# Kernel optimization log

Hardware: AMD Instinct MI355X
Metric: run time of the kernel (lower is better)

## Reference

```python
import jax, jax.numpy as jnp
import numpy as np

N_POINTS = 1 << 20
N_LEVELS = 16
F_PER_LVL = 2
LOG2_T = 19
T = 1 << LOG2_T
BASE_RES = 16
PER_LEVEL_SCALE = float(np.exp2(np.log2(2048.0 / 16.0) / (N_LEVELS - 1)))
# 8 trilinear corner offsets [8,3]
OFFSETS = np.stack(np.meshgrid(*([np.array([0, 1])] * 3), indexing='ij'), axis=-1).reshape(8, 3)
PRIMES = np.array([1, 2654435761, 805459861], dtype=np.uint32)  # tcnn spatial hash primes


def _level_params(l):
    # tcnn: grid_scale = 2^(l*log2(s)) * base - 1 ; resolution = ceil(scale)+1
    scale = np.exp2(l * np.log2(PER_LEVEL_SCALE)) * BASE_RES - 1.0
    res = int(np.ceil(scale)) + 1
    return float(scale), res


def hash_encode(x, table):
    """x: [N,3] in [0,1]; table: [L,T,F]. Returns [N, L*F]."""
    offs = jnp.asarray(OFFSETS)                     # [8,3] int32
    primes = jnp.asarray(PRIMES)                    # [3] uint32
    feats = []
    for l in range(N_LEVELS):
        scale, res = _level_params(l)
        pos = x * scale + 0.5                       # [N,3]
        pos_grid = jnp.floor(pos)
        w = pos - pos_grid                          # [N,3] interp weights
        c0 = pos_grid.astype(jnp.int32)             # [N,3]
        corners = c0[None, :, :] + offs[:, None, :]  # [8,N,3]
        if res ** 3 <= T:
            # dense indexing for coarse levels (fits in hashmap)
            cc = jnp.clip(corners, 0, res - 1)
            idx = cc[..., 0] + cc[..., 1] * res + cc[..., 2] * (res * res)
        else:
            cu = corners.astype(jnp.uint32)
            h = (cu[..., 0] * primes[0]) ^ (cu[..., 1] * primes[1]) ^ (cu[..., 2] * primes[2])
            idx = (h & jnp.uint32(T - 1)).astype(jnp.int32)
        f = table[l][idx]                           # [8,N,F] gather
        # trilinear weights: prod over dims of (w if corner bit else 1-w)
        wc = jnp.prod(jnp.where(offs[:, None, :] == 1, w[None], 1.0 - w[None]), axis=-1)  # [8,N]
        feats.append(jnp.sum(wc[..., None] * f, axis=0))  # [N,F]
    return jnp.concatenate(feats, axis=-1)          # [N, 32]


def _softplus10(z):
    return jax.nn.softplus(10.0 * z) / 10.0


def setup_inputs() -> dict:
    key = jax.random.key(0)
    k = jax.random.split(key, 6)
    x = jax.random.uniform(k[0], (N_POINTS, 3), dtype=jnp.float32)
    table = jax.random.normal(k[1], (N_LEVELS, T, F_PER_LVL), dtype=jnp.float32) * 1e-2
    w1 = jax.random.normal(k[2], (64, 32), dtype=jnp.float32) * 0.1
    w2 = jax.random.normal(k[3], (64, 64), dtype=jnp.float32) * 0.1
    w3 = jax.random.normal(k[4], (64, 64), dtype=jnp.float32) * 0.1
    w4 = jax.random.normal(k[5], (1, 64), dtype=jnp.float32) * 0.1
    return {"x": x, "table": table, "w1": w1, "w2": w2, "w3": w3, "w4": w4}


def reference(x, table, w1, w2, w3, w4):
    enc = hash_encode(x, table)                     # [N,32]
    h = _softplus10(enc @ w1.T)
    h = _softplus10(h @ w2.T)
    h = _softplus10(h @ w3.T)
    sdf = h @ w4.T                                  # [N,1]
    return sdf
```

## Files before the change

kernel.cpp:

```cpp
#include <hip/hip_runtime.h>
#include <cmath>

#define T_SIZE (1u << 19)
#define CB 512
#define NBLK 128
#define RCAP 3584

typedef _Float16 h8 __attribute__((ext_vector_type(8)));
typedef _Float16 h4 __attribute__((ext_vector_type(4)));
typedef _Float16 h2 __attribute__((ext_vector_type(2)));
typedef float f4 __attribute__((ext_vector_type(4)));

struct Levels {
    float scale[16];
    int   res[16];
    unsigned dense_mask;
};

__device__ __forceinline__ float softplus10(float z) {
    float e = __builtin_amdgcn_exp2f(fminf(z * 14.426950408889634f, 126.0f));
    return __builtin_amdgcn_logf(1.0f + e) * 0.069314718055994531f;
}

__global__ __launch_bounds__(256) void convert_kernel(
    const float2* __restrict__ t, h2* __restrict__ o, int total4,
    const float* __restrict__ w1, const float* __restrict__ w2,
    const float* __restrict__ w3, _Float16* __restrict__ wh)
{
    int i = blockIdx.x * 256 + threadIdx.x;
    if (i < total4) {
        const float2* src = t + (size_t)i * 4;
        h8 r;
#pragma unroll
        for (int j = 0; j < 4; ++j) {
            float2 v = src[j];
            r[2 * j]     = (_Float16)v.x;
            r[2 * j + 1] = (_Float16)v.y;
        }
        *(h8*)(o + (size_t)i * 4) = r;
    } else {
        int k = i - total4;
        if (k < 10240) {
            float v = (k < 2048) ? w1[k] : (k < 6144) ? w2[k - 2048] : w3[k - 6144];
            wh[k] = (_Float16)v;
        }
    }
}

__device__ __forceinline__ unsigned spread3(unsigned v) {
    v &= 1023u;
    v = (v | (v << 16)) & 0x030000FFu;
    v = (v | (v << 8))  & 0x0300F00Fu;
    v = (v | (v << 4))  & 0x030C30C3u;
    v = (v | (v << 2))  & 0x09249249u;
    return v;
}

__device__ __forceinline__ unsigned morton_key(float px, float py, float pz) {
    unsigned qx = (unsigned)fminf(fmaxf(px, 0.f) * 32.f, 31.f);
    unsigned qy = (unsigned)fminf(fmaxf(py, 0.f) * 32.f, 31.f);
    unsigned qz = (unsigned)fminf(fmaxf(pz, 0.f) * 32.f, 31.f);
    return (spread3(qx) << 2) | (spread3(qy) << 1) | spread3(qz);
}

__global__ __launch_bounds__(256) void hist_kernel(
    const float* __restrict__ xs, unsigned* __restrict__ M, int N)
{
    __shared__ unsigned h[CB];
    for (int t = threadIdx.x; t < CB; t += 256) h[t] = 0u;
    __syncthreads();
    const int per = N / NBLK;
    const int s = blockIdx.x * per;
    for (int i = s + threadIdx.x; i < s + per; i += 256) {
        unsigned k = morton_key(xs[3 * i], xs[3 * i + 1], xs[3 * i + 2]) >> 6;
        atomicAdd(&h[k], 1u);
    }
    __syncthreads();
    for (int t = threadIdx.x; t < CB; t += 256)
        M[t * NBLK + blockIdx.x] = h[t];
}

__global__ __launch_bounds__(1024) void scan_kernel(
    const unsigned* __restrict__ M, unsigned* __restrict__ Ms)
{
    __shared__ unsigned tmp[1024];
    const int t = threadIdx.x;
    const int PER = (CB * NBLK) / 1024;
    unsigned s = 0;
    for (int j = 0; j < PER; ++j) s += M[t * PER + j];
    tmp[t] = s;
    __syncthreads();
    for (int d = 1; d < 1024; d <<= 1) {
        unsigned v = (t >= d) ? tmp[t - d] : 0u;
        __syncthreads();
        tmp[t] += v;
        __syncthreads();
    }
    unsigned run = (t > 0) ? tmp[t - 1] : 0u;
    for (int j = 0; j < PER; ++j) {
        unsigned v = M[t * PER + j];
        Ms[t * PER + j] = run;
        run += v;
    }
}

__global__ __launch_bounds__(256) void cscatter_kernel(
    const float* __restrict__ xs, const unsigned* __restrict__ Ms,
    float4* __restrict__ sx4, int N)
{
    __shared__ unsigned cur[CB];
    for (int t = threadIdx.x; t < CB; t += 256)
        cur[t] = Ms[t * NBLK + blockIdx.x];
    __syncthreads();
    const int per = N / NBLK;
    const int s = blockIdx.x * per;
    for (int i = s + threadIdx.x; i < s + per; i += 256) {
        float px = xs[3 * i], py = xs[3 * i + 1], pz = xs[3 * i + 2];
        unsigned k = morton_key(px, py, pz) >> 6;
        unsigned pos = atomicAdd(&cur[k], 1u);
        sx4[pos] = make_float4(px, py, pz, __uint_as_float((unsigned)i));
    }
}

__global__ __launch_bounds__(256) void refine_kernel(
    float4* __restrict__ sx4, const unsigned* __restrict__ Ms, int N)
{
    __shared__ float4 pts[RCAP];
    __shared__ unsigned h[64], base[64];
    const int b = blockIdx.x;
    const unsigned s = Ms[b * NBLK];
    const unsigned e = (b == CB - 1) ? (unsigned)N : Ms[(b + 1) * NBLK];
    const unsigned cnt = e - s;
    if (cnt > RCAP) return;
    if (threadIdx.x < 64) h[threadIdx.x] = 0u;
    __syncthreads();
    for (unsigned i = threadIdx.x; i < cnt; i += 256) {
        float4 q = sx4[s + i];
        pts[i] = q;
        unsigned k = morton_key(q.x, q.y, q.z) & 63u;
        atomicAdd(&h[k], 1u);
    }
    __syncthreads();
    if (threadIdx.x == 0) {
        unsigned a = 0;
        for (int j = 0; j < 64; ++j) { base[j] = a; a += h[j]; }
    }
    __syncthreads();
    if (threadIdx.x < 64) h[threadIdx.x] = 0u;
    __syncthreads();
    for (unsigned i = threadIdx.x; i < cnt; i += 256) {
        float4 q = pts[i];
        unsigned k = morton_key(q.x, q.y, q.z) & 63u;
        unsigned r = base[k] + atomicAdd(&h[k], 1u);
        sx4[s + r] = q;
    }
}

__device__ __forceinline__ void gather_pair(
    const h2* __restrict__ tl, unsigned i0, unsigned i1,
    float2& v0, float2& v1)
{
    unsigned g = i0 & ~3u;
    union { h8 v; uint4 u; } cv;
    cv.v = *(const h8*)(tl + g);
    unsigned p0 = i0 & 3u;
    unsigned a01 = (p0 & 1u) ? cv.u.y : cv.u.x;
    unsigned a23 = (p0 & 1u) ? cv.u.w : cv.u.z;
    unsigned e0  = (p0 & 2u) ? a23 : a01;
    unsigned e1;
    if ((i1 & ~3u) == g) {
        unsigned p1 = i1 & 3u;
        unsigned b01 = (p1 & 1u) ? cv.u.y : cv.u.x;
        unsigned b23 = (p1 & 1u) ? cv.u.w : cv.u.z;
        e1 = (p1 & 2u) ? b23 : b01;
    } else {
        e1 = *(const unsigned*)(tl + i1);
    }
    h2 c0 = __builtin_bit_cast(h2, e0);
    h2 c1 = __builtin_bit_cast(h2, e1);
    v0 = make_float2((float)c0[0], (float)c0[1]);
    v1 = make_float2((float)c1[0], (float)c1[1]);
}

__device__ __forceinline__ h2 encode_point(
    float px, float py, float pz, float s, int res, bool dense,
    const h2* __restrict__ tl)
{
    float fx = px * s + 0.5f, fy = py * s + 0.5f, fz = pz * s + 0.5f;
    float gx = floorf(fx), gy = floorf(fy), gz = floorf(fz);
    float wx = fx - gx, wy = fy - gy, wz = fz - gz;
    int cx = (int)gx, cy = (int)gy, cz = (int)gz;

    float2 vx0[4], vx1[4];
    if (dense) {
        int r1 = res - 1;
        int x0 = min(cx, r1), x1 = min(cx + 1, r1);
        int y0 = min(cy, r1), y1 = min(cy + 1, r1);
        int z0 = min(cz, r1), z1 = min(cz + 1, r1);
        int rr = res * res;
        int bases[4] = {y0 * res + z0 * rr, y0 * res + z1 * rr,
                        y1 * res + z0 * rr, y1 * res + z1 * rr};
#pragma unroll
        for (int j = 0; j < 4; ++j)
            gather_pair(tl, (unsigned)(x0 + bases[j]), (unsigned)(x1 + bases[j]),
                        vx0[j], vx1[j]);
    } else {
        unsigned hy0 = (unsigned)cy * 2654435761u, hy1 = (unsigned)(cy + 1) * 2654435761u;
        unsigned hz0 = (unsigned)cz * 805459861u,  hz1 = (unsigned)(cz + 1) * 805459861u;
        unsigned Y[4] = {hy0 ^ hz0, hy0 ^ hz1, hy1 ^ hz0, hy1 ^ hz1};
        const unsigned M = T_SIZE - 1;
#pragma unroll
        for (int j = 0; j < 4; ++j)
            gather_pair(tl, ((unsigned)cx ^ Y[j]) & M,
                        ((unsigned)(cx + 1) ^ Y[j]) & M, vx0[j], vx1[j]);
    }

    float wx0 = 1.f - wx, wy0 = 1.f - wy, wz0 = 1.f - wz;
    float wyz[4] = {wy0 * wz0, wy0 * wz, wy * wz0, wy * wz};
    float f0 = 0.f, f1 = 0.f;
#pragma unroll
    for (int j = 0; j < 4; ++j) {
        float w0 = wx0 * wyz[j], w1 = wx * wyz[j];
        f0 += w0 * vx0[j].x + w1 * vx1[j].x;
        f1 += w0 * vx0[j].y + w1 * vx1[j].y;
    }
    h2 r; r[0] = (_Float16)f0; r[1] = (_Float16)f1;
    return r;
}

__global__ __launch_bounds__(256) void encode_kernel(
    const float* __restrict__ xs, const h2* __restrict__ table,
    h2* __restrict__ enc2, Levels lv, int lbase, int N)
{
    __shared__ float sx[768];
    const int i0 = blockIdx.x * 256;
    for (int t = threadIdx.x; t < 768; t += 256) sx[t] = xs[(size_t)i0 * 3 + t];
    __syncthreads();

    const int l = lbase + blockIdx.y;
    const int i = i0 + threadIdx.x;
    if (i >= N) return;
    h2 r = encode_point(sx[threadIdx.x * 3], sx[threadIdx.x * 3 + 1],
                        sx[threadIdx.x * 3 + 2], lv.scale[l], lv.res[l],
                        (lv.dense_mask >> l) & 1u, table + (size_t)l * T_SIZE);
    enc2[(size_t)l * N + i] = r;
}

__global__ __launch_bounds__(256) void encode_kernel_sorted(
    const float4* __restrict__ xs4, const h2* __restrict__ table,
    h2* __restrict__ enc2, Levels lv, int lbase, int N)
{
    const int i = blockIdx.x * 256 + threadIdx.x;
    if (i >= N) return;
    const int l = lbase + blockIdx.y;
    float4 q = xs4[i];
    h2 r = encode_point(q.x, q.y, q.z, lv.scale[l], lv.res[l],
                        (lv.dense_mask >> l) & 1u, table + (size_t)l * T_SIZE);
    enc2[(size_t)l * N + i] = r;
}

template <typename WT>
__device__ __forceinline__ h8 load_frag8(const WT* p) {
    if constexpr (sizeof(WT) == 2) {
        return *(const h8*)p;
    } else {
        h8 r;
#pragma unroll
        for (int j = 0; j < 8; ++j) r[j] = (_Float16)p[j];
        return r;
    }
}

template <typename WT, bool LOCAL, bool SORTED>
__global__ __launch_bounds__(256, 3) void fused_kernel(
    const float* __restrict__ xs, const float4* __restrict__ xs4,
    const h2* __restrict__ table16, const h2* __restrict__ enc2,
    const WT* __restrict__ w1, const WT* __restrict__ w2,
    const WT* __restrict__ w3, const float* __restrict__ w4,
    float* __restrict__ out, Levels lv, int N)
{
    constexpr int AR = 72;
    __shared__ __align__(16) char smem[4 * 9216];
    __shared__ float sx[768];

    const int tid  = threadIdx.x;
    const int wave = tid >> 6;
    const int lane = tid & 63;
    const int lrow = lane & 15;
    const int quad = lane >> 4;
    const int base = blockIdx.x * 256;
    char* wmem = smem + wave * 9216;
    const f4 zero = {0.f, 0.f, 0.f, 0.f};

    float px, py, pz;
    unsigned oi = 0;
    if constexpr (SORTED) {
        float4 q = xs4[base + tid];
        px = q.x; py = q.y; pz = q.z;
        oi = __float_as_uint(q.w);
    } else {
        for (int t = tid; t < 768; t += 256) sx[t] = xs[(size_t)base * 3 + t];
        __syncthreads();
        px = sx[tid * 3]; py = sx[tid * 3 + 1]; pz = sx[tid * 3 + 2];
    }
    const int p = tid & 63;

    if (LOCAL) {
#pragma unroll
        for (int l = 5; l < 15; ++l) {
            h2 v = enc2[(size_t)l * N + base + tid];
            *(h2*)(wmem + ((l >> 2) << 10) + (p << 4) + ((l & 3) << 2)) = v;
        }
        const int LMAP[6] = {0, 1, 2, 3, 4, 15};
#pragma unroll 2
        for (int s6 = 0; s6 < 6; ++s6) {
            const int l = LMAP[s6];
            h2 v = encode_point(px, py, pz, lv.scale[l], lv.res[l],
                                (lv.dense_mask >> l) & 1u,
                                table16 + (size_t)l * T_SIZE);
            *(h2*)(wmem + ((l >> 2) << 10) + (p << 4) + ((l & 3) << 2)) = v;
        }
    } else {
#pragma unroll
        for (int l = 0; l < 16; ++l) {
            h2 v = enc2[(size_t)l * N + base + tid];
            *(h2*)(wmem + ((l >> 2) << 10) + (p << 4) + ((l & 3) << 2)) = v;
        }
    }

    asm volatile("" ::: "memory");

    h8 aW1[4];
#pragma unroll
    for (int tm = 0; tm < 4; ++tm)
        aW1[tm] = load_frag8(w1 + (tm * 16 + lrow) * 32 + quad * 8);
    h8 aW2[4][2], aW3[4][2];
#pragma unroll
    for (int tm = 0; tm < 4; ++tm)
#pragma unroll
        for (int km = 0; km < 2; ++km) {
            aW2[tm][km] = load_frag8(w2 + (tm * 16 + lrow) * 64 + km * 32 + quad * 8);
            aW3[tm][km] = load_frag8(w3 + (tm * 16 + lrow) * 64 + km * 32 + quad * 8);
        }
    h4 w4q[4];
#pragma unroll
    for (int tm = 0; tm < 4; ++tm)
#pragma unroll
        for (int r = 0; r < 4; ++r) w4q[tm][r] = (_Float16)w4[tm * 16 + quad * 4 + r];

    h8 bin[4];
#pragma unroll
    for (int t = 0; t < 4; ++t)
        bin[t] = *(const h8*)(wmem + (quad << 10) + ((t * 16 + lrow) << 4));

    _Float16* wAct = (_Float16*)wmem;

#pragma unroll
    for (int t = 0; t < 4; ++t) {
        const int arow = (t * 16 + lrow) * AR;
#pragma unroll
        for (int tm = 0; tm < 4; ++tm) {
            f4 acc = __builtin_amdgcn_mfma_f32_16x16x32_f16(aW1[tm], bin[t], zero, 0, 0, 0);
            h4 pk;
#pragma unroll
            for (int r = 0; r < 4; ++r) pk[r] = (_Float16)softplus10(acc[r]);
            *(h4*)&wAct[arow + tm * 16 + quad * 4] = pk;
        }
    }

#pragma unroll
    for (int t = 0; t < 4; ++t) {
        const int arow = (t * 16 + lrow) * AR;
        h8 b0 = *(const h8*)&wAct[arow + quad * 8];
        h8 b1 = *(const h8*)&wAct[arow + 32 + quad * 8];
        f4 accs[4];
#pragma unroll
        for (int tm = 0; tm < 4; ++tm) {
            f4 acc = __builtin_amdgcn_mfma_f32_16x16x32_f16(aW2[tm][0], b0, zero, 0, 0, 0);
            acc     = __builtin_amdgcn_mfma_f32_16x16x32_f16(aW2[tm][1], b1, acc,  0, 0, 0);
            accs[tm] = acc;
        }
#pragma unroll
        for (int tm = 0; tm < 4; ++tm) {
            h4 pk;
#pragma unroll
            for (int r = 0; r < 4; ++r) pk[r] = (_Float16)softplus10(accs[tm][r]);
            *(h4*)&wAct[arow + tm * 16 + quad * 4] = pk;
        }
    }

#pragma unroll
    for (int t = 0; t < 4; ++t) {
        const int arow = (t * 16 + lrow) * AR;
        h8 b0 = *(const h8*)&wAct[arow + quad * 8];
        h8 b1 = *(const h8*)&wAct[arow + 32 + quad * 8];
        float sum = 0.f;
#pragma unroll
        for (int tm = 0; tm < 4; ++tm) {
            f4 acc = __builtin_amdgcn_mfma_f32_16x16x32_f16(aW3[tm][0], b0, zero, 0, 0, 0);
            acc     = __builtin_amdgcn_mfma_f32_16x16x32_f16(aW3[tm][1], b1, acc,  0, 0, 0);
#pragma unroll
            for (int r = 0; r < 4; ++r)
                sum += (float)w4q[tm][r] * softplus10(acc[r]);
        }
        sum += __shfl_xor(sum, 16, 64);
        sum += __shfl_xor(sum, 32, 64);
        if constexpr (SORTED) {
            unsigned t_oi = __shfl(oi, t * 16 + lrow, 64);
            if (quad == 0) out[t_oi] = sum;
        } else {
            if (quad == 0)
                out[base + wave * 64 + t * 16 + lrow] = sum;
        }
    }
}

__global__ __launch_bounds__(256) void encode_kernel_f32(
    const float* __restrict__ xs, const float2* __restrict__ table,
    h2* __restrict__ enc2, Levels lv, int N)
{
    const int i = blockIdx.x * 256 + threadIdx.x;
    const int l = blockIdx.y;
    if (i >= N) return;
    float px = xs[3 * i], py = xs[3 * i + 1], pz = xs[3 * i + 2];
    float s = lv.scale[l];
    int res = lv.res[l];
    float fx = px * s + 0.5f, fy = py * s + 0.5f, fz = pz * s + 0.5f;
    float gx = floorf(fx), gy = floorf(fy), gz = floorf(fz);
    float wx = fx - gx, wy = fy - gy, wz = fz - gz;
    int cx = (int)gx, cy = (int)gy, cz = (int)gz;
    unsigned idx[8];
    if ((lv.dense_mask >> l) & 1u) {
        int r1 = res - 1;
        int x0 = min(cx, r1), x1 = min(cx + 1, r1);
        int y0 = min(cy, r1), y1 = min(cy + 1, r1);
        int z0 = min(cz, r1), z1 = min(cz + 1, r1);
        int rr = res * res;
        idx[0] = x0 + y0 * res + z0 * rr; idx[1] = x0 + y0 * res + z1 * rr;
        idx[2] = x0 + y1 * res + z0 * rr; idx[3] = x0 + y1 * res + z1 * rr;
        idx[4] = x1 + y0 * res + z0 * rr; idx[5] = x1 + y0 * res + z1 * rr;
        idx[6] = x1 + y1 * res + z0 * rr; idx[7] = x1 + y1 * res + z1 * rr;
    } else {
        unsigned hx0 = (unsigned)cx, hx1 = (unsigned)(cx + 1);
        unsigned hy0 = (unsigned)cy * 2654435761u, hy1 = (unsigned)(cy + 1) * 2654435761u;
        unsigned hz0 = (unsigned)cz * 805459861u,  hz1 = (unsigned)(cz + 1) * 805459861u;
        idx[0] = (hx0^hy0^hz0) & (T_SIZE-1); idx[1] = (hx0^hy0^hz1) & (T_SIZE-1);
        idx[2] = (hx0^hy1^hz0) & (T_SIZE-1); idx[3] = (hx0^hy1^hz1) & (T_SIZE-1);
        idx[4] = (hx1^hy0^hz0) & (T_SIZE-1); idx[5] = (hx1^hy0^hz1) & (T_SIZE-1);
        idx[6] = (hx1^hy1^hz0) & (T_SIZE-1); idx[7] = (hx1^hy1^hz1) & (T_SIZE-1);
    }
    const float2* tl = table + (size_t)l * T_SIZE;
    float wx0 = 1.f - wx, wy0 = 1.f - wy, wz0 = 1.f - wz;
    float wcs[8] = {wx0*wy0*wz0, wx0*wy0*wz, wx0*wy*wz0, wx0*wy*wz,
                    wx*wy0*wz0,  wx*wy0*wz,  wx*wy*wz0,  wx*wy*wz};
    float f0 = 0.f, f1 = 0.f;
#pragma unroll
    for (int c = 0; c < 8; ++c) {
        float2 v = tl[idx[c]];
        f0 += wcs[c] * v.x; f1 += wcs[c] * v.y;
    }
    h2 r; r[0] = (_Float16)f0; r[1] = (_Float16)f1;
    enc2[(size_t)l * N + i] = r;
}

extern "C" void kernel_launch(void* const* d_in, const int* in_sizes, int n_in,
                              void* d_out, int out_size, void* d_ws, size_t ws_size,
                              hipStream_t stream) {
    const float* x     = (const float*)d_in[0];
    const float* table = (const float*)d_in[1];
    const float* w1    = (const float*)d_in[2];
    const float* w2    = (const float*)d_in[3];
    const float* w3    = (const float*)d_in[4];
    const float* w4    = (const float*)d_in[5];
    float* out = (float*)d_out;
    const int N = in_sizes[0] / 3;

    Levels lv;
    lv.dense_mask = 0;
    const double pls = exp2(log2(2048.0 / 16.0) / 15.0);
    const double lg  = log2(pls);
    for (int l = 0; l < 16; ++l) {
        double sc = exp2((double)l * lg) * 16.0 - 1.0;
        int res = (int)ceil(sc) + 1;
        lv.scale[l] = (float)sc;
        lv.res[l]   = res;
        if ((long long)res * res * res <= (long long)T_SIZE) lv.dense_mask |= (1u << l);
    }

    const size_t encBytes   = (size_t)16 * N * 4;
    const size_t tableBytes = (size_t)16 * T_SIZE * 4;
    const size_t whBytes    = 32768;
    const size_t sx4Bytes   = (size_t)N * 16;
    const size_t mBytes     = (size_t)CB * NBLK * 4;
    h2* enc2 = (h2*)d_ws;

    const int ptBlocks = (N + 255) / 256;

    if (ws_size >= encBytes + tableBytes + whBytes + sx4Bytes + 2 * mBytes
        && (N % NBLK) == 0) {
        h2* table16    = (h2*)((char*)d_ws + encBytes);
        _Float16* wh   = (_Float16*)((char*)d_ws + encBytes + tableBytes);
        float4* sx4    = (float4*)((char*)d_ws + encBytes + tableBytes + whBytes);
        unsigned* M    = (unsigned*)((char*)d_ws + encBytes + tableBytes + whBytes + sx4Bytes);
        unsigned* Ms   = M + (size_t)CB * NBLK;

        const int total4 = 16 * T_SIZE / 4;
        const int convBlocks = (total4 + 10240 + 255) / 256;
        hipLaunchKernelGGL(convert_kernel, dim3(convBlocks), dim3(256), 0, stream,
                           (const float2*)table, table16, total4, w1, w2, w3, wh);

        hipLaunchKernelGGL(hist_kernel, dim3(NBLK), dim3(256), 0, stream, x, M, N);
        hipLaunchKernelGGL(scan_kernel, dim3(1), dim3(1024), 0, stream, M, Ms);
        hipLaunchKernelGGL(cscatter_kernel, dim3(NBLK), dim3(256), 0, stream,
                           x, Ms, sx4, N);
        hipLaunchKernelGGL(refine_kernel, dim3(CB), dim3(256), 0, stream,
                           sx4, Ms, N);

        hipLaunchKernelGGL(encode_kernel_sorted, dim3(ptBlocks, 10), dim3(256), 0, stream,
                           (const float4*)sx4, (const h2*)table16, enc2, lv, 5, N);
        hipLaunchKernelGGL((fused_kernel<_Float16, true, true>), dim3(ptBlocks), dim3(256),
                           0, stream, x, (const float4*)sx4, (const h2*)table16,
                           (const h2*)enc2, wh, wh + 2048, wh + 6144, w4, out, lv, N);
    } else if (ws_size >= encBytes + tableBytes + whBytes) {
        h2* table16 = (h2*)((char*)d_ws + encBytes);
        _Float16* wh = (_Float16*)((char*)d_ws + encBytes + tableBytes);
        const int total4 = 16 * T_SIZE / 4;
        const int convBlocks = (total4 + 10240 + 255) / 256;
        hipLaunchKernelGGL(convert_kernel, dim3(convBlocks), dim3(256), 0, stream,
                           (const float2*)table, table16, total4, w1, w2, w3, wh);
        hipLaunchKernelGGL(encode_kernel, dim3(ptBlocks, 10), dim3(256), 0, stream,
                           x, (const h2*)table16, enc2, lv, 5, N);
        hipLaunchKernelGGL((fused_kernel<_Float16, true, false>), dim3(ptBlocks), dim3(256),
                           0, stream, x, (const float4*)nullptr, (const h2*)table16,
                           (const h2*)enc2, wh, wh + 2048, wh + 6144, w4, out, lv, N);
    } else {
        hipLaunchKernelGGL(encode_kernel_f32, dim3(ptBlocks, 16), dim3(256), 0, stream,
                           x, (const float2*)table, enc2, lv, N);
        hipLaunchKernelGGL((fused_kernel<float, false, false>), dim3(ptBlocks), dim3(256),
                           0, stream, x, (const float4*)nullptr, (const h2*)nullptr,
                           (const h2*)enc2, w1, w2, w3, w4, out, lv, N);
    }
}
```

Before: 451.6 us.

## Fuse histogram into convert kernel and stage coarse scatter through LDS

New measurement: 481.3 us. 1.07x slower.

```diff
diff --git a/kernel.cpp b/kernel.cpp
--- a/kernel.cpp
+++ b/kernel.cpp
@@ -3,7 +3,7 @@
 
 #define T_SIZE (1u << 19)
 #define CB 512
-#define NBLK 128
+#define NBLK 512
 #define RCAP 3584
 
 typedef _Float16 h8 __attribute__((ext_vector_type(8)));
@@ -20,31 +20,6 @@
 __device__ __forceinline__ float softplus10(float z) {
     float e = __builtin_amdgcn_exp2f(fminf(z * 14.426950408889634f, 126.0f));
     return __builtin_amdgcn_logf(1.0f + e) * 0.069314718055994531f;
-}
-
-__global__ __launch_bounds__(256) void convert_kernel(
-    const float2* __restrict__ t, h2* __restrict__ o, int total4,
-    const float* __restrict__ w1, const float* __restrict__ w2,
-    const float* __restrict__ w3, _Float16* __restrict__ wh)
-{
-    int i = blockIdx.x * 256 + threadIdx.x;
-    if (i < total4) {
-        const float2* src = t + (size_t)i * 4;
-        h8 r;
-#pragma unroll
-        for (int j = 0; j < 4; ++j) {
-            float2 v = src[j];
-            r[2 * j]     = (_Float16)v.x;
-            r[2 * j + 1] = (_Float16)v.y;
-        }
-        *(h8*)(o + (size_t)i * 4) = r;
-    } else {
-        int k = i - total4;
-        if (k < 10240) {
-            float v = (k < 2048) ? w1[k] : (k < 6144) ? w2[k - 2048] : w3[k - 6144];
-            wh[k] = (_Float16)v;
-        }
-    }
 }
 
 __device__ __forceinline__ unsigned spread3(unsigned v) {
@@ -63,31 +38,58 @@
     return (spread3(qx) << 2) | (spread3(qy) << 1) | spread3(qz);
 }
 
-__global__ __launch_bounds__(256) void hist_kernel(
-    const float* __restrict__ xs, unsigned* __restrict__ M, int N)
-{
-    __shared__ unsigned h[CB];
-    for (int t = threadIdx.x; t < CB; t += 256) h[t] = 0u;
-    __syncthreads();
-    const int per = N / NBLK;
-    const int s = blockIdx.x * per;
-    for (int i = s + threadIdx.x; i < s + per; i += 256) {
-        unsigned k = morton_key(xs[3 * i], xs[3 * i + 1], xs[3 * i + 2]) >> 6;
-        atomicAdd(&h[k], 1u);
-    }
-    __syncthreads();
-    for (int t = threadIdx.x; t < CB; t += 256)
-        M[t * NBLK + blockIdx.x] = h[t];
+__global__ __launch_bounds__(256) void convert_kernel(
+    const float2* __restrict__ t, h2* __restrict__ o, int total4,
+    const float* __restrict__ w1, const float* __restrict__ w2,
+    const float* __restrict__ w3, _Float16* __restrict__ wh,
+    const float* __restrict__ xs, unsigned short* __restrict__ M, int N)
+{
+    const int histStart = (total4 + 10240 + 255) >> 8;
+    if ((int)blockIdx.x >= histStart) {
+        __shared__ unsigned h[CB];
+        const int blk = blockIdx.x - histStart;
+        for (int t2 = threadIdx.x; t2 < CB; t2 += 256) h[t2] = 0u;
+        __syncthreads();
+        const int s = blk * 2048;
+#pragma unroll
+        for (int j = 0; j < 8; ++j) {
+            int i = s + threadIdx.x + j * 256;
+            unsigned k = morton_key(xs[3 * i], xs[3 * i + 1], xs[3 * i + 2]) >> 6;
+            atomicAdd(&h[k], 1u);
+        }
+        __syncthreads();
+        for (int t2 = threadIdx.x; t2 < CB; t2 += 256)
+            M[t2 * NBLK + blk] = (unsigned short)h[t2];
+        return;
+    }
+    int i = blockIdx.x * 256 + threadIdx.x;
+    if (i < total4) {
+        const float2* src = t + (size_t)i * 4;
+        h8 r;
+#pragma unroll
+        for (int j = 0; j < 4; ++j) {
+            float2 v = src[j];
+            r[2 * j]     = (_Float16)v.x;
+            r[2 * j + 1] = (_Float16)v.y;
+        }
+        *(h8*)(o + (size_t)i * 4) = r;
+    } else {
+        int k = i - total4;
+        if (k < 10240) {
+            float v = (k < 2048) ? w1[k] : (k < 6144) ? w2[k - 2048] : w3[k - 6144];
+            wh[k] = (_Float16)v;
+        }
+    }
 }
 
 __global__ __launch_bounds__(1024) void scan_kernel(
-    const unsigned* __restrict__ M, unsigned* __restrict__ Ms)
+    const unsigned short* __restrict__ M, unsigned* __restrict__ Ms)
 {
     __shared__ unsigned tmp[1024];
     const int t = threadIdx.x;
-    const int PER = (CB * NBLK) / 1024;
+    const int PERS = (CB * NBLK) / 1024;
     unsigned s = 0;
-    for (int j = 0; j < PER; ++j) s += M[t * PER + j];
+    for (int j = 0; j < PERS; ++j) s += M[t * PERS + j];
     tmp[t] = s;
     __syncthreads();
     for (int d = 1; d < 1024; d <<= 1) {
@@ -97,9 +99,9 @@
         __syncthreads();
     }
     unsigned run = (t > 0) ? tmp[t - 1] : 0u;
-    for (int j = 0; j < PER; ++j) {
-        unsigned v = M[t * PER + j];
-        Ms[t * PER + j] = run;
+    for (int j = 0; j < PERS; ++j) {
+        unsigned v = M[t * PERS + j];
+        Ms[t * PERS + j] = run;
         run += v;
     }
 }
@@ -108,18 +110,53 @@
     const float* __restrict__ xs, const unsigned* __restrict__ Ms,
     float4* __restrict__ sx4, int N)
 {
-    __shared__ unsigned cur[CB];
-    for (int t = threadIdx.x; t < CB; t += 256)
-        cur[t] = Ms[t * NBLK + blockIdx.x];
-    __syncthreads();
-    const int per = N / NBLK;
-    const int s = blockIdx.x * per;
-    for (int i = s + threadIdx.x; i < s + per; i += 256) {
+    __shared__ float4  pts[2048];
+    __shared__ unsigned gp[2048];
+    __shared__ unsigned lh[CB];
+    __shared__ unsigned lbase[CB];
+    __shared__ unsigned tmp[256];
+    const int tid = threadIdx.x;
+    const int blk = blockIdx.x;
+    for (int t2 = tid; t2 < CB; t2 += 256) lh[t2] = 0u;
+    __syncthreads();
+    const int s = blk * 2048;
+    float4  myp[8];
+    unsigned myk[8];
+#pragma unroll
+    for (int j = 0; j < 8; ++j) {
+        int i = s + tid + j * 256;
         float px = xs[3 * i], py = xs[3 * i + 1], pz = xs[3 * i + 2];
-        unsigned k = morton_key(px, py, pz) >> 6;
-        unsigned pos = atomicAdd(&cur[k], 1u);
-        sx4[pos] = make_float4(px, py, pz, __uint_as_float((unsigned)i));
-    }
+        myp[j] = make_float4(px, py, pz, __uint_as_float((unsigned)i));
+        myk[j] = morton_key(px, py, pz) >> 6;
+        atomicAdd(&lh[myk[j]], 1u);
+    }
+    __syncthreads();
+    unsigned a0 = lh[2 * tid], a1 = lh[2 * tid + 1];
+    tmp[tid] = a0 + a1;
+    __syncthreads();
+    for (int d = 1; d < 256; d <<= 1) {
+        unsigned v = (tid >= d) ? tmp[tid - d] : 0u;
+        __syncthreads();
+        tmp[tid] += v;
+        __syncthreads();
+    }
+    unsigned eb = (tid > 0) ? tmp[tid - 1] : 0u;
+    lbase[2 * tid] = eb;
+    lbase[2 * tid + 1] = eb + a0;
+    __syncthreads();
+    lh[2 * tid] = 0u; lh[2 * tid + 1] = 0u;
+    __syncthreads();
+#pragma unroll
+    for (int j = 0; j < 8; ++j) {
+        unsigned k = myk[j];
+        unsigned r = atomicAdd(&lh[k], 1u);
+        unsigned slot = lbase[k] + r;
+        pts[slot] = myp[j];
+        gp[slot] = Ms[k * NBLK + blk] + r;
+    }
+    __syncthreads();
+    for (int j = tid; j < 2048; j += 256)
+        sx4[gp[j]] = pts[j];
 }
 
 __global__ __launch_bounds__(256) void refine_kernel(
@@ -160,20 +197,13 @@
     const h2* __restrict__ tl, unsigned i0, unsigned i1,
     float2& v0, float2& v1)
 {
-    unsigned g = i0 & ~3u;
-    union { h8 v; uint4 u; } cv;
-    cv.v = *(const h8*)(tl + g);
-    unsigned p0 = i0 & 3u;
-    unsigned a01 = (p0 & 1u) ? cv.u.y : cv.u.x;
-    unsigned a23 = (p0 & 1u) ? cv.u.w : cv.u.z;
-    unsigned e0  = (p0 & 2u) ? a23 : a01;
-    unsigned e1;
-    if ((i1 & ~3u) == g) {
-        unsigned p1 = i1 & 3u;
-        unsigned b01 = (p1 & 1u) ? cv.u.y : cv.u.x;
-        unsigned b23 = (p1 & 1u) ? cv.u.w : cv.u.z;
-        e1 = (p1 & 2u) ? b23 : b01;
-    } else {
+    unsigned e0, e1;
+    if ((i0 ^ i1) == 1u) {
+        uint2 both = *(const uint2*)(tl + (i0 & ~1u));
+        e0 = (i0 & 1u) ? both.y : both.x;
+        e1 = (i0 & 1u) ? both.x : both.y;
+    } else {
+        e0 = *(const unsigned*)(tl + i0);
         e1 = *(const unsigned*)(tl + i1);
     }
     h2 c0 = __builtin_bit_cast(h2, e0);
@@ -491,25 +521,23 @@
     const size_t tableBytes = (size_t)16 * T_SIZE * 4;
     const size_t whBytes    = 32768;
     const size_t sx4Bytes   = (size_t)N * 16;
-    const size_t mBytes     = (size_t)CB * NBLK * 4;
     h2* enc2 = (h2*)d_ws;
 
     const int ptBlocks = (N + 255) / 256;
 
-    if (ws_size >= encBytes + tableBytes + whBytes + sx4Bytes + 2 * mBytes
-        && (N % NBLK) == 0) {
+    if (ws_size >= encBytes + tableBytes + whBytes + sx4Bytes
+        && N == NBLK * 2048) {
         h2* table16    = (h2*)((char*)d_ws + encBytes);
         _Float16* wh   = (_Float16*)((char*)d_ws + encBytes + tableBytes);
         float4* sx4    = (float4*)((char*)d_ws + encBytes + tableBytes + whBytes);
-        unsigned* M    = (unsigned*)((char*)d_ws + encBytes + tableBytes + whBytes + sx4Bytes);
-        unsigned* Ms   = M + (size_t)CB * NBLK;
+        unsigned short* M = (unsigned short*)d_ws;
+        unsigned* Ms      = (unsigned*)((char*)d_ws + 1024 * 1024);
 
         const int total4 = 16 * T_SIZE / 4;
         const int convBlocks = (total4 + 10240 + 255) / 256;
-        hipLaunchKernelGGL(convert_kernel, dim3(convBlocks), dim3(256), 0, stream,
-                           (const float2*)table, table16, total4, w1, w2, w3, wh);
-
-        hipLaunchKernelGGL(hist_kernel, dim3(NBLK), dim3(256), 0, stream, x, M, N);
+        hipLaunchKernelGGL(convert_kernel, dim3(convBlocks + NBLK), dim3(256), 0,
+                           stream, (const float2*)table, table16, total4,
+                           w1, w2, w3, wh, x, M, N);
         hipLaunchKernelGGL(scan_kernel, dim3(1), dim3(1024), 0, stream, M, Ms);
         hipLaunchKernelGGL(cscatter_kernel, dim3(NBLK), dim3(256), 0, stream,
                            x, Ms, sx4, N);
@@ -527,7 +555,8 @@
         const int total4 = 16 * T_SIZE / 4;
         const int convBlocks = (total4 + 10240 + 255) / 256;
         hipLaunchKernelGGL(convert_kernel, dim3(convBlocks), dim3(256), 0, stream,
-                           (const float2*)table, table16, total4, w1, w2, w3, wh);
+                           (const float2*)table, table16, total4, w1, w2, w3, wh,
+                           x, (unsigned short*)nullptr, N);
         hipLaunchKernelGGL(encode_kernel, dim3(ptBlocks, 10), dim3(256), 0, stream,
                            x, (const h2*)table16, enc2, lv, 5, N);
         hipLaunchKernelGGL((fused_kernel<_Float16, true, false>), dim3(ptBlocks), dim3(256),
```

## Fuse histogram into convert kernel and move levels 5-9 encoding into fused kernel

Applied to the files above, without the earlier changes.

After: 450.6 us. About the same (-0.2%).

```diff
diff --git a/kernel.cpp b/kernel.cpp
--- a/kernel.cpp
+++ b/kernel.cpp
@@ -20,31 +20,6 @@
 __device__ __forceinline__ float softplus10(float z) {
     float e = __builtin_amdgcn_exp2f(fminf(z * 14.426950408889634f, 126.0f));
     return __builtin_amdgcn_logf(1.0f + e) * 0.069314718055994531f;
-}
-
-__global__ __launch_bounds__(256) void convert_kernel(
-    const float2* __restrict__ t, h2* __restrict__ o, int total4,
-    const float* __restrict__ w1, const float* __restrict__ w2,
-    const float* __restrict__ w3, _Float16* __restrict__ wh)
-{
-    int i = blockIdx.x * 256 + threadIdx.x;
-    if (i < total4) {
-        const float2* src = t + (size_t)i * 4;
-        h8 r;
-#pragma unroll
-        for (int j = 0; j < 4; ++j) {
-            float2 v = src[j];
-            r[2 * j]     = (_Float16)v.x;
-            r[2 * j + 1] = (_Float16)v.y;
-        }
-        *(h8*)(o + (size_t)i * 4) = r;
-    } else {
-        int k = i - total4;
-        if (k < 10240) {
-            float v = (k < 2048) ? w1[k] : (k < 6144) ? w2[k - 2048] : w3[k - 6144];
-            wh[k] = (_Float16)v;
-        }
-    }
 }
 
 __device__ __forceinline__ unsigned spread3(unsigned v) {
@@ -63,21 +38,47 @@
     return (spread3(qx) << 2) | (spread3(qy) << 1) | spread3(qz);
 }
 
-__global__ __launch_bounds__(256) void hist_kernel(
+__global__ __launch_bounds__(256) void convert_kernel(
+    const float2* __restrict__ t, h2* __restrict__ o, int total4,
+    const float* __restrict__ w1, const float* __restrict__ w2,
+    const float* __restrict__ w3, _Float16* __restrict__ wh,
     const float* __restrict__ xs, unsigned* __restrict__ M, int N)
 {
-    __shared__ unsigned h[CB];
-    for (int t = threadIdx.x; t < CB; t += 256) h[t] = 0u;
-    __syncthreads();
-    const int per = N / NBLK;
-    const int s = blockIdx.x * per;
-    for (int i = s + threadIdx.x; i < s + per; i += 256) {
-        unsigned k = morton_key(xs[3 * i], xs[3 * i + 1], xs[3 * i + 2]) >> 6;
-        atomicAdd(&h[k], 1u);
-    }
-    __syncthreads();
-    for (int t = threadIdx.x; t < CB; t += 256)
-        M[t * NBLK + blockIdx.x] = h[t];
+    const int histStart = (total4 + 10240 + 255) >> 8;
+    if ((int)blockIdx.x >= histStart) {
+        __shared__ unsigned h[CB];
+        const int blk = blockIdx.x - histStart;
+        for (int t2 = threadIdx.x; t2 < CB; t2 += 256) h[t2] = 0u;
+        __syncthreads();
+        const int per = N / NBLK;
+        const int s = blk * per;
+        for (int i = s + threadIdx.x; i < s + per; i += 256) {
+            unsigned k = morton_key(xs[3 * i], xs[3 * i + 1], xs[3 * i + 2]) >> 6;
+            atomicAdd(&h[k], 1u);
+        }
+        __syncthreads();
+        for (int t2 = threadIdx.x; t2 < CB; t2 += 256)
+            M[t2 * NBLK + blk] = h[t2];
+        return;
+    }
+    int i = blockIdx.x * 256 + threadIdx.x;
+    if (i < total4) {
+        const float2* src = t + (size_t)i * 4;
+        h8 r;
+#pragma unroll
+        for (int j = 0; j < 4; ++j) {
+            float2 v = src[j];
+            r[2 * j]     = (_Float16)v.x;
+            r[2 * j + 1] = (_Float16)v.y;
+        }
+        *(h8*)(o + (size_t)i * 4) = r;
+    } else {
+        int k = i - total4;
+        if (k < 10240) {
+            float v = (k < 2048) ? w1[k] : (k < 6144) ? w2[k - 2048] : w3[k - 6144];
+            wh[k] = (_Float16)v;
+        }
+    }
 }
 
 __global__ __launch_bounds__(1024) void scan_kernel(
@@ -307,13 +308,13 @@
 
     if (LOCAL) {
 #pragma unroll
-        for (int l = 5; l < 15; ++l) {
+        for (int l = 10; l < 15; ++l) {
             h2 v = enc2[(size_t)l * N + base + tid];
             *(h2*)(wmem + ((l >> 2) << 10) + (p << 4) + ((l & 3) << 2)) = v;
         }
-        const int LMAP[6] = {0, 1, 2, 3, 4, 15};
-#pragma unroll 2
-        for (int s6 = 0; s6 < 6; ++s6) {
+        const int LMAP[11] = {15, 5, 6, 7, 8, 9, 0, 1, 2, 3, 4};
+#pragma unroll
+        for (int s6 = 0; s6 < 11; ++s6) {
             const int l = LMAP[s6];
             h2 v = encode_point(px, py, pz, lv.scale[l], lv.res[l],
                                 (lv.dense_mask >> l) & 1u,
@@ -491,33 +492,32 @@
     const size_t tableBytes = (size_t)16 * T_SIZE * 4;
     const size_t whBytes    = 32768;
     const size_t sx4Bytes   = (size_t)N * 16;
-    const size_t mBytes     = (size_t)CB * NBLK * 4;
     h2* enc2 = (h2*)d_ws;
 
     const int ptBlocks = (N + 255) / 256;
 
-    if (ws_size >= encBytes + tableBytes + whBytes + sx4Bytes + 2 * mBytes
-        && (N % NBLK) == 0) {
+    if (ws_size >= encBytes + tableBytes + whBytes + sx4Bytes
+        && N == NBLK * 8192) {
         h2* table16    = (h2*)((char*)d_ws + encBytes);
         _Float16* wh   = (_Float16*)((char*)d_ws + encBytes + tableBytes);
         float4* sx4    = (float4*)((char*)d_ws + encBytes + tableBytes + whBytes);
-        unsigned* M    = (unsigned*)((char*)d_ws + encBytes + tableBytes + whBytes + sx4Bytes);
-        unsigned* Ms   = M + (size_t)CB * NBLK;
+        unsigned* M  = (unsigned*)d_ws;
+        unsigned* Ms = (unsigned*)((char*)d_ws + 512 * 1024);
 
         const int total4 = 16 * T_SIZE / 4;
         const int convBlocks = (total4 + 10240 + 255) / 256;
-        hipLaunchKernelGGL(convert_kernel, dim3(convBlocks), dim3(256), 0, stream,
-                           (const float2*)table, table16, total4, w1, w2, w3, wh);
-
-        hipLaunchKernelGGL(hist_kernel, dim3(NBLK), dim3(256), 0, stream, x, M, N);
+        hipLaunchKernelGGL(convert_kernel, dim3(convBlocks + NBLK), dim3(256), 0,
+                           stream, (const float2*)table, table16, total4,
+                           w1, w2, w3, wh, x, M, N);
         hipLaunchKernelGGL(scan_kernel, dim3(1), dim3(1024), 0, stream, M, Ms);
         hipLaunchKernelGGL(cscatter_kernel, dim3(NBLK), dim3(256), 0, stream,
                            x, Ms, sx4, N);
         hipLaunchKernelGGL(refine_kernel, dim3(CB), dim3(256), 0, stream,
                            sx4, Ms, N);
 
-        hipLaunchKernelGGL(encode_kernel_sorted, dim3(ptBlocks, 10), dim3(256), 0, stream,
-                           (const float4*)sx4, (const h2*)table16, enc2, lv, 5, N);
+        hipLaunchKernelGGL(encode_kernel_sorted, dim3(ptBlocks, 5), dim3(256),
+                           0, stream, (const float4*)sx4, (const h2*)table16,
+                           enc2, lv, 10, N);
         hipLaunchKernelGGL((fused_kernel<_Float16, true, true>), dim3(ptBlocks), dim3(256),
                            0, stream, x, (const float4*)sx4, (const h2*)table16,
                            (const h2*)enc2, wh, wh + 2048, wh + 6144, w4, out, lv, N);
@@ -527,9 +527,10 @@
         const int total4 = 16 * T_SIZE / 4;
         const int convBlocks = (total4 + 10240 + 255) / 256;
         hipLaunchKernelGGL(convert_kernel, dim3(convBlocks), dim3(256), 0, stream,
-                           (const float2*)table, table16, total4, w1, w2, w3, wh);
-        hipLaunchKernelGGL(encode_kernel, dim3(ptBlocks, 10), dim3(256), 0, stream,
-                           x, (const h2*)table16, enc2, lv, 5, N);
+                           (const float2*)table, table16, total4, w1, w2, w3, wh,
+                           x, (unsigned*)nullptr, N);
+        hipLaunchKernelGGL(encode_kernel, dim3(ptBlocks, 5), dim3(256), 0, stream,
+                           x, (const h2*)table16, enc2, lv, 10, N);
         hipLaunchKernelGGL((fused_kernel<_Float16, true, false>), dim3(ptBlocks), dim3(256),
                            0, stream, x, (const float4*)nullptr, (const h2*)table16,
                            (const h2*)enc2, wh, wh + 2048, wh + 6144, w4, out, lv, N);
```
